# Kernel tuning notes

Hardware: AMD Instinct MI355X
Metric: run time of the kernel (lower is better)

The kernel has to match this reference:

```python
import jax, jax.numpy as jnp
import numpy as np
import math

D = 2048            # fc_feat_size (hardcoded sqrt(2048) scale in source)
IMAGES = 20         # images_per_person
NEIGHBOR = 5        # neighbor_size (sliding window width)
T = IMAGES - NEIGHBOR + 1   # number of windows = 16
SCALE = 1.0 / math.sqrt(2048.0)


def _attention(x, Wq, bq, Wk, bk, Wv, bv):
    # x: [N, L, D] -> [N, L, D]; bmm-softmax-bmm as in source
    q = x @ Wq.T + bq
    k = x @ Wk.T + bk
    v = x @ Wv.T + bv
    dot = jnp.einsum('nld,nmd->nlm', q, k) * SCALE
    w = jax.nn.softmax(dot, axis=-1)
    return jnp.einsum('nlm,nmd->nld', w, v)


def _lstm_final(x, Wih, Whh, bih, bhh):
    # PyTorch-convention LSTM (gates i,f,g,o); x: [N, L, D] -> final hidden [N, H]
    N = x.shape[0]
    H = Whh.shape[1]
    xg = x @ Wih.T + (bih + bhh)   # [N, L, 4H] precompute input projections

    def step(carry, xt):
        h, c = carry
        gates = xt + h @ Whh.T
        i, f, g, o = jnp.split(gates, 4, axis=-1)
        c = jax.nn.sigmoid(f) * c + jax.nn.sigmoid(i) * jnp.tanh(g)
        h = jax.nn.sigmoid(o) * jnp.tanh(c)
        return (h, c), None

    init = (jnp.zeros((N, H), x.dtype), jnp.zeros((N, H), x.dtype))
    (h, _), _ = jax.lax.scan(step, init, jnp.swapaxes(xg, 0, 1))
    return h


def _layernorm(x, g, b, eps=1e-5):
    mu = jnp.mean(x, axis=-1, keepdims=True)
    var = jnp.var(x, axis=-1, keepdims=True)
    return (x - mu) * jax.lax.rsqrt(var + eps) * g + b


def setup_inputs() -> dict:
    key = jax.random.key(0)
    ks = iter(jax.random.split(key, 32))
    s = 0.02
    p = {}
    p['fc_feats'] = jax.random.normal(next(ks), (64, IMAGES, D), jnp.float32)
    for pre in ('nsa', 'sa'):
        for nm in ('Wq', 'Wk', 'Wv'):
            p[f'{pre}_{nm}'] = jax.random.normal(next(ks), (D, D), jnp.float32) * s
        for nm in ('bq', 'bk', 'bv'):
            p[f'{pre}_{nm}'] = jnp.zeros((D,), jnp.float32)
        p[f'{pre}_Wih'] = jax.random.normal(next(ks), (4 * D, D), jnp.float32) * s
        p[f'{pre}_Whh'] = jax.random.normal(next(ks), (4 * D, D), jnp.float32) * s
        p[f'{pre}_bih'] = jnp.zeros((4 * D,), jnp.float32)
        p[f'{pre}_bhh'] = jnp.zeros((4 * D,), jnp.float32)
    p['ln_g'] = jnp.ones((D,), jnp.float32)
    p['ln_b'] = jnp.zeros((D,), jnp.float32)
    return p


def reference(fc_feats,
              nsa_Wq, nsa_Wk, nsa_Wv, nsa_bq, nsa_bk, nsa_bv,
              nsa_Wih, nsa_Whh, nsa_bih, nsa_bhh,
              sa_Wq, sa_Wk, sa_Wv, sa_bq, sa_bk, sa_bv,
              sa_Wih, sa_Whh, sa_bih, sa_bhh,
              ln_g, ln_b):
    B = fc_feats.shape[0]
    # Sliding windows: window t covers images [t, t+NEIGHBOR) -> [B, T, W, D]
    idx = jnp.arange(T)[:, None] + jnp.arange(NEIGHBOR)[None, :]
    windows = fc_feats[:, idx]                       # [B, T, W, D]
    wflat = windows.reshape(B * T, NEIGHBOR, D)
    # NeighboringSelfAttention: attention within window + LSTM final state
    att = _attention(wflat, nsa_Wq, nsa_bq, nsa_Wk, nsa_bk, nsa_Wv, nsa_bv)
    nsa = _lstm_final(att, nsa_Wih, nsa_Whh, nsa_bih, nsa_bhh)  # [B*T, D]
    nsa_feats = nsa.reshape(B, T, D)
    new_nsa_feats = _layernorm(nsa_feats, ln_g, ln_b)
    # SelfAttention over the T window summaries + LSTM final state
    att2 = _attention(new_nsa_feats, sa_Wq, sa_bq, sa_Wk, sa_bk, sa_Wv, sa_bv)
    sa_feats = _lstm_final(att2, sa_Wih, sa_Whh, sa_bih, sa_bhh)  # [B, D]
    return (sa_feats, new_nsa_feats)
```

## Files before the change

kernel.cpp:

```cpp
#include <hip/hip_runtime.h>
#include <hip/hip_bf16.h>

typedef unsigned int  u32;
typedef unsigned short u16;

typedef __bf16 bf16x8 __attribute__((ext_vector_type(8)));
typedef float  f32x4  __attribute__((ext_vector_type(4)));

#define D2048 2048
#define SCALE 0.022097086912079612f

__device__ __forceinline__ u32 f2bfbits(float f) {
    u32 u = __float_as_uint(f);
    return (u + 0x7FFFu + ((u >> 16) & 1u)) >> 16;
}
__device__ __forceinline__ u32 pack2(float a, float b) {
    return f2bfbits(a) | (f2bfbits(b) << 16);
}
__device__ __forceinline__ float bf2f(u32 h) {
    return __uint_as_float(h << 16);
}
__device__ __forceinline__ void unpack8(uint4 v, float* f) {
    f[0] = bf2f(v.x & 0xFFFFu); f[1] = bf2f(v.x >> 16);
    f[2] = bf2f(v.y & 0xFFFFu); f[3] = bf2f(v.y >> 16);
    f[4] = bf2f(v.z & 0xFFFFu); f[5] = bf2f(v.z >> 16);
    f[6] = bf2f(v.w & 0xFFFFu); f[7] = bf2f(v.w >> 16);
}
__device__ __forceinline__ float sigmf(float x) { return 1.f / (1.f + __expf(-x)); }
__device__ __forceinline__ float tanhf_(float x) {
    x = fminf(15.f, fmaxf(-15.f, x));
    float e = __expf(2.f * x);
    return (e - 1.f) / (e + 1.f);
}

__device__ __forceinline__ void gload_lds16(const u16* g, u16* l) {
    __builtin_amdgcn_global_load_lds(
        (const __attribute__((address_space(1))) unsigned int*)g,
        (__attribute__((address_space(3))) unsigned int*)l,
        16, 0, 0);
}

struct CvtArgs {
    const float* src[8];
    u16*         dst[8];
    int          n4[8];
    int          nseg;
};
__global__ __launch_bounds__(256) void cvt_multi(CvtArgs a) {
    int stride = gridDim.x * 256;
    for (int s = 0; s < a.nseg; ++s) {
        const float4* S = reinterpret_cast<const float4*>(a.src[s]);
        uint2*        D = reinterpret_cast<uint2*>(a.dst[s]);
        int n4 = a.n4[s];
        for (int i = blockIdx.x * 256 + threadIdx.x; i < n4; i += stride) {
            float4 v = S[i];
            uint2 p;
            p.x = pack2(v.x, v.y);
            p.y = pack2(v.z, v.w);
            D[i] = p;
        }
    }
}

template <bool QKV3, bool HAS_BIAS, bool OUT_BF16>
__global__ __launch_bounds__(256) void gemm_bt(const u16* __restrict__ A, int lda,
                                               const u16* __restrict__ B0,
                                               const u16* __restrict__ B1,
                                               const u16* __restrict__ B2,
                                               const float* __restrict__ bias0,
                                               const float* __restrict__ bias1,
                                               const float* __restrict__ bias2,
                                               void* __restrict__ Cout,
                                               size_t zCstride,
                                               int M, int N, int K) {
    __shared__ u16 Abuf[2][128 * 64];
    __shared__ u16 Bbuf[2][128 * 64];

    const int tid  = threadIdx.x;
    const int lane = tid & 63;
    const int wave = tid >> 6;
    const int wr   = (wave >> 1) * 64;
    const int wc   = (wave & 1) * 64;
    const int rowBase = blockIdx.y * 128;
    const int colBase = blockIdx.x * 128;
    const int l15 = lane & 15, l4 = lane >> 4;
    const int srow = lane >> 3;
    const int scol = (lane & 7) * 8;

    const u16* B = B0;
    const float* bias = bias0;
    void* C = Cout;
    if (QKV3) {
        int z = blockIdx.z;
        B    = (z == 0) ? B0 : ((z == 1) ? B1 : B2);
        bias = (z == 0) ? bias0 : ((z == 1) ? bias1 : bias2);
        C    = OUT_BF16 ? (void*)((u16*)Cout + (size_t)z * zCstride)
                        : (void*)((float*)Cout + (size_t)z * zCstride);
    }

    const u16* ga = A + (size_t)(rowBase + wave * 32 + srow) * lda + scol;
    const u16* gb = B + (size_t)(colBase + wave * 32 + srow) * K + scol;
    const int ldsOff = (wave * 32) * 64;

    f32x4 acc[4][4];
#pragma unroll
    for (int i = 0; i < 4; i++)
#pragma unroll
        for (int j = 0; j < 4; j++) acc[i][j] = f32x4{0.f, 0.f, 0.f, 0.f};

    const int nt = K >> 6;

#pragma unroll
    for (int i = 0; i < 4; ++i) {
        gload_lds16(ga + (size_t)(i * 8) * lda, &Abuf[0][ldsOff + i * 8 * 64]);
        gload_lds16(gb + (size_t)(i * 8) * K,   &Bbuf[0][ldsOff + i * 8 * 64]);
    }

    for (int t = 0; t < nt; ++t) {
        const int cur = t & 1;
        if (t + 1 < nt) {
            const int k1 = (t + 1) << 6;
#pragma unroll
            for (int i = 0; i < 4; ++i) {
                gload_lds16(ga + (size_t)(i * 8) * lda + k1,
                            &Abuf[cur ^ 1][ldsOff + i * 8 * 64]);
                gload_lds16(gb + (size_t)(i * 8) * K + k1,
                            &Bbuf[cur ^ 1][ldsOff + i * 8 * 64]);
            }
            asm volatile("s_waitcnt vmcnt(8)" ::: "memory");
        } else {
            asm volatile("s_waitcnt vmcnt(0)" ::: "memory");
        }
        __builtin_amdgcn_s_barrier();
        __builtin_amdgcn_sched_barrier(0);
#pragma unroll
        for (int kk = 0; kk < 2; ++kk) {
            bf16x8 af[4], bfr[4];
#pragma unroll
            for (int i = 0; i < 4; i++) {
                af[i]  = *reinterpret_cast<const bf16x8*>(
                    &Abuf[cur][(wr + i * 16 + l15) * 64 + kk * 32 + l4 * 8]);
                bfr[i] = *reinterpret_cast<const bf16x8*>(
                    &Bbuf[cur][(wc + i * 16 + l15) * 64 + kk * 32 + l4 * 8]);
            }
#pragma unroll
            for (int i = 0; i < 4; i++)
#pragma unroll
                for (int j = 0; j < 4; j++)
                    acc[i][j] = __builtin_amdgcn_mfma_f32_16x16x32_bf16(af[i], bfr[j],
                                                                        acc[i][j], 0, 0, 0);
        }
        __builtin_amdgcn_sched_barrier(0);
        __builtin_amdgcn_s_barrier();
    }

#pragma unroll
    for (int i = 0; i < 4; i++) {
        int row0 = rowBase + wr + i * 16 + l4 * 4;
#pragma unroll
        for (int j = 0; j < 4; j++) {
            int col = colBase + wc + j * 16 + l15;
            float bv = HAS_BIAS ? bias[col] : 0.f;
#pragma unroll
            for (int rr = 0; rr < 4; rr++) {
                float val = acc[i][j][rr] + bv;
                if (OUT_BF16)
                    ((u16*)C)[(size_t)(row0 + rr) * N + col] = (u16)f2bfbits(val);
                else
                    ((float*)C)[(size_t)(row0 + rr) * N + col] = val;
            }
        }
    }
}

__global__ __launch_bounds__(256) void gemm_skinny64(const u16* __restrict__ A,
                                                     const u16* __restrict__ B,
                                                     float* __restrict__ part,
                                                     int N, int K) {
    __shared__ u16 Abuf[2][64 * 64];
    __shared__ u16 Bbuf[2][128 * 64];
    const int tid = threadIdx.x, lane = tid & 63, wave = tid >> 6;
    const int colBase = blockIdx.x * 128;
    const int kp = blockIdx.y;
    const int kseg = K >> 2;
    const int kBeg = kp * kseg;
    const int l15 = lane & 15, l4 = lane >> 4;
    const int srow = lane >> 3, scol = (lane & 7) * 8;

    const u16* ga = A + (size_t)(wave * 16 + srow) * K + scol + kBeg;
    const u16* gb = B + (size_t)(colBase + wave * 32 + srow) * K + scol + kBeg;
    const int laOff = (wave * 16) * 64;
    const int lbOff = (wave * 32) * 64;

    f32x4 acc[4][2];
#pragma unroll
    for (int i = 0; i < 4; i++)
#pragma unroll
        for (int j = 0; j < 2; j++) acc[i][j] = f32x4{0.f, 0.f, 0.f, 0.f};

    const int nt = kseg >> 6;

#pragma unroll
    for (int i = 0; i < 2; ++i)
        gload_lds16(ga + (size_t)(i * 8) * K, &Abuf[0][laOff + i * 8 * 64]);
#pragma unroll
    for (int i = 0; i < 4; ++i)
        gload_lds16(gb + (size_t)(i * 8) * K, &Bbuf[0][lbOff + i * 8 * 64]);

    for (int t = 0; t < nt; ++t) {
        const int cur = t & 1;
        if (t + 1 < nt) {
            const int k1 = (t + 1) << 6;
#pragma unroll
            for (int i = 0; i < 2; ++i)
                gload_lds16(ga + (size_t)(i * 8) * K + k1, &Abuf[cur ^ 1][laOff + i * 8 * 64]);
#pragma unroll
            for (int i = 0; i < 4; ++i)
                gload_lds16(gb + (size_t)(i * 8) * K + k1, &Bbuf[cur ^ 1][lbOff + i * 8 * 64]);
            asm volatile("s_waitcnt vmcnt(6)" ::: "memory");
        } else {
            asm volatile("s_waitcnt vmcnt(0)" ::: "memory");
        }
        __builtin_amdgcn_s_barrier();
        __builtin_amdgcn_sched_barrier(0);
#pragma unroll
        for (int kk = 0; kk < 2; ++kk) {
            bf16x8 af[4], bfr[2];
#pragma unroll
            for (int i = 0; i < 4; i++)
                af[i] = *reinterpret_cast<const bf16x8*>(
                    &Abuf[cur][(i * 16 + l15) * 64 + kk * 32 + l4 * 8]);
#pragma unroll
            for (int j = 0; j < 2; j++)
                bfr[j] = *reinterpret_cast<const bf16x8*>(
                    &Bbuf[cur][(wave * 32 + j * 16 + l15) * 64 + kk * 32 + l4 * 8]);
#pragma unroll
            for (int i = 0; i < 4; i++)
#pragma unroll
                for (int j = 0; j < 2; j++)
                    acc[i][j] = __builtin_amdgcn_mfma_f32_16x16x32_bf16(af[i], bfr[j],
                                                                        acc[i][j], 0, 0, 0);
        }
        __builtin_amdgcn_sched_barrier(0);
        __builtin_amdgcn_s_barrier();
    }

    float* cp = part + (size_t)kp * 64 * N;
#pragma unroll
    for (int i = 0; i < 4; i++) {
        int row0 = i * 16 + l4 * 4;
#pragma unroll
        for (int j = 0; j < 2; j++) {
            int col = colBase + wave * 32 + j * 16 + l15;
#pragma unroll
            for (int rr = 0; rr < 4; rr++)
                cp[(size_t)(row0 + rr) * N + col] = acc[i][j][rr];
        }
    }
}

__global__ __launch_bounds__(256) void attn_win5(const u16* __restrict__ q0,
                                                 const u16* __restrict__ k0,
                                                 const u16* __restrict__ v0,
                                                 u16* __restrict__ att) {
    int n = blockIdx.x;
    int b = n >> 4, t = n & 15;
    int tid = threadIdx.x, lane = tid & 63, wave = tid >> 6;
    int d0 = tid * 8;
    size_t base = (size_t)(b * 20 + t) * D2048;

    float qv[5][8];
#pragma unroll
    for (int i = 0; i < 5; i++) {
        uint4 v = *reinterpret_cast<const uint4*>(q0 + base + (size_t)i * D2048 + d0);
        unpack8(v, qv[i]);
    }
    float part[25];
#pragma unroll
    for (int p = 0; p < 25; p++) part[p] = 0.f;
#pragma unroll
    for (int m = 0; m < 5; m++) {
        float kv[8];
        uint4 v = *reinterpret_cast<const uint4*>(k0 + base + (size_t)m * D2048 + d0);
        unpack8(v, kv);
#pragma unroll
        for (int l = 0; l < 5; l++)
#pragma unroll
            for (int j = 0; j < 8; j++) part[l * 5 + m] += qv[l][j] * kv[j];
    }
#pragma unroll
    for (int p = 0; p < 25; p++) {
        float s = part[p];
#pragma unroll
        for (int msk = 32; msk; msk >>= 1) s += __shfl_xor(s, msk, 64);
        part[p] = s;
    }
    __shared__ float wred[4][25];
    __shared__ float wmat[25];
    if (lane == 0) {
#pragma unroll
        for (int p = 0; p < 25; p++) wred[wave][p] = part[p];
    }
    __syncthreads();
    if (tid < 5) {
        int l = tid;
        float dv[5], mx = -1e30f;
#pragma unroll
        for (int m = 0; m < 5; m++) {
            dv[m] = (wred[0][l * 5 + m] + wred[1][l * 5 + m] + wred[2][l * 5 + m] +
                     wred[3][l * 5 + m]) * SCALE;
            mx = fmaxf(mx, dv[m]);
        }
        float ssum = 0.f;
#pragma unroll
        for (int m = 0; m < 5; m++) { dv[m] = __expf(dv[m] - mx); ssum += dv[m]; }
        float inv = 1.f / ssum;
#pragma unroll
        for (int m = 0; m < 5; m++) wmat[l * 5 + m] = dv[m] * inv;
    }
    __syncthreads();

    float oacc[5][8];
#pragma unroll
    for (int l = 0; l < 5; l++)
#pragma unroll
        for (int j = 0; j < 8; j++) oacc[l][j] = 0.f;
#pragma unroll
    for (int m = 0; m < 5; m++) {
        float vv[8];
        uint4 v = *reinterpret_cast<const uint4*>(v0 + base + (size_t)m * D2048 + d0);
        unpack8(v, vv);
#pragma unroll
        for (int l = 0; l < 5; l++) {
            float w = wmat[l * 5 + m];
#pragma unroll
            for (int j = 0; j < 8; j++) oacc[l][j] += w * vv[j];
        }
    }
#pragma unroll
    for (int l = 0; l < 5; l++) {
        uint4 p;
        p.x = pack2(oacc[l][0], oacc[l][1]);
        p.y = pack2(oacc[l][2], oacc[l][3]);
        p.z = pack2(oacc[l][4], oacc[l][5]);
        p.w = pack2(oacc[l][6], oacc[l][7]);
        *reinterpret_cast<uint4*>(att + (size_t)(n * 5 + l) * D2048 + d0) = p;
    }
}

__global__ __launch_bounds__(256) void attn_seq16(const u16* __restrict__ q2,
                                                  const u16* __restrict__ k2,
                                                  const u16* __restrict__ v2,
                                                  u16* __restrict__ att2) {
    int r = blockIdx.x;
    int b = r >> 4;
    int tid = threadIdx.x, lane = tid & 63, wave = tid >> 6;
    int d0 = tid * 8;
    size_t kbase = (size_t)b * 16 * D2048;

    float qv[8];
    {
        uint4 v = *reinterpret_cast<const uint4*>(q2 + (size_t)r * D2048 + d0);
        unpack8(v, qv);
    }
    float part[16];
#pragma unroll
    for (int m = 0; m < 16; m++) part[m] = 0.f;
#pragma unroll
    for (int m = 0; m < 16; m++) {
        float kv[8];
        uint4 v = *reinterpret_cast<const uint4*>(k2 + kbase + (size_t)m * D2048 + d0);
        unpack8(v, kv);
#pragma unroll
        for (int j = 0; j < 8; j++) part[m] += qv[j] * kv[j];
    }
#pragma unroll
    for (int m = 0; m < 16; m++) {
        float s = part[m];
#pragma unroll
        for (int msk = 32; msk; msk >>= 1) s += __shfl_xor(s, msk, 64);
        part[m] = s;
    }
    __shared__ float wred[4][16];
    __shared__ float wmat[16];
    if (lane == 0) {
#pragma unroll
        for (int m = 0; m < 16; m++) wred[wave][m] = part[m];
    }
    __syncthreads();
    if (tid == 0) {
        float dv[16], mx = -1e30f;
#pragma unroll
        for (int m = 0; m < 16; m++) {
            dv[m] = (wred[0][m] + wred[1][m] + wred[2][m] + wred[3][m]) * SCALE;
            mx = fmaxf(mx, dv[m]);
        }
        float ssum = 0.f;
#pragma unroll
        for (int m = 0; m < 16; m++) { dv[m] = __expf(dv[m] - mx); ssum += dv[m]; }
        float inv = 1.f / ssum;
#pragma unroll
        for (int m = 0; m < 16; m++) wmat[m] = dv[m] * inv;
    }
    __syncthreads();

    float oacc[8];
#pragma unroll
    for (int j = 0; j < 8; j++) oacc[j] = 0.f;
#pragma unroll
    for (int m = 0; m < 16; m++) {
        float vv[8];
        uint4 v = *reinterpret_cast<const uint4*>(v2 + kbase + (size_t)m * D2048 + d0);
        unpack8(v, vv);
        float w = wmat[m];
#pragma unroll
        for (int j = 0; j < 8; j++) oacc[j] += w * vv[j];
    }
    uint4 p;
    p.x = pack2(oacc[0], oacc[1]);
    p.y = pack2(oacc[2], oacc[3]);
    p.z = pack2(oacc[4], oacc[5]);
    p.w = pack2(oacc[6], oacc[7]);
    *reinterpret_cast<uint4*>(att2 + (size_t)r * D2048 + d0) = p;
}

template <int NPARTS>
__global__ __launch_bounds__(256) void lstm_gate(const u16* __restrict__ xg,
                                                 int xg_stride,
                                                 const float* __restrict__ hW,
                                                 const float* __restrict__ bih,
                                                 const float* __restrict__ bhh,
                                                 float* __restrict__ c,
                                                 float* __restrict__ h,
                                                 u16* __restrict__ hbf,
                                                 float* __restrict__ hout,
                                                 int rows) {
    int idx = blockIdx.x * 256 + threadIdx.x;
    int total = rows * 512;
    if (idx >= total) return;
    int n  = idx >> 9;
    int j4 = (idx & 511) * 4;

    const u16* xr = xg + (size_t)n * xg_stride + j4;
    float4 gi, gf, gg, go;
    {
        uint2 ri = *reinterpret_cast<const uint2*>(xr);
        uint2 rf = *reinterpret_cast<const uint2*>(xr + 2048);
        uint2 rg = *reinterpret_cast<const uint2*>(xr + 4096);
        uint2 ro = *reinterpret_cast<const uint2*>(xr + 6144);
        gi = {bf2f(ri.x & 0xFFFFu), bf2f(ri.x >> 16), bf2f(ri.y & 0xFFFFu), bf2f(ri.y >> 16)};
        gf = {bf2f(rf.x & 0xFFFFu), bf2f(rf.x >> 16), bf2f(rf.y & 0xFFFFu), bf2f(rf.y >> 16)};
        gg = {bf2f(rg.x & 0xFFFFu), bf2f(rg.x >> 16), bf2f(rg.y & 0xFFFFu), bf2f(rg.y >> 16)};
        go = {bf2f(ro.x & 0xFFFFu), bf2f(ro.x >> 16), bf2f(ro.y & 0xFFFFu), bf2f(ro.y >> 16)};
    }

    float4 bi1 = *reinterpret_cast<const float4*>(bih + j4);
    float4 bf1 = *reinterpret_cast<const float4*>(bih + 2048 + j4);
    float4 bg1 = *reinterpret_cast<const float4*>(bih + 4096 + j4);
    float4 bo1 = *reinterpret_cast<const float4*>(bih + 6144 + j4);
    float4 bi2 = *reinterpret_cast<const float4*>(bhh + j4);
    float4 bf2_ = *reinterpret_cast<const float4*>(bhh + 2048 + j4);
    float4 bg2 = *reinterpret_cast<const float4*>(bhh + 4096 + j4);
    float4 bo2 = *reinterpret_cast<const float4*>(bhh + 6144 + j4);

    gi.x += bi1.x + bi2.x; gi.y += bi1.y + bi2.y; gi.z += bi1.z + bi2.z; gi.w += bi1.w + bi2.w;
    gf.x += bf1.x + bf2_.x; gf.y += bf1.y + bf2_.y; gf.z += bf1.z + bf2_.z; gf.w += bf1.w + bf2_.w;
    gg.x += bg1.x + bg2.x; gg.y += bg1.y + bg2.y; gg.z += bg1.z + bg2.z; gg.w += bg1.w + bg2.w;
    go.x += bo1.x + bo2.x; go.y += bo1.y + bo2.y; go.z += bo1.z + bo2.z; go.w += bo1.w + bo2.w;

#pragma unroll
    for (int p = 0; p < NPARTS; ++p) {
        const float* hr = hW + (size_t)p * 524288 + (size_t)n * 8192;
        float4 hi = *reinterpret_cast<const float4*>(hr + j4);
        float4 hf = *reinterpret_cast<const float4*>(hr + 2048 + j4);
        float4 hg = *reinterpret_cast<const float4*>(hr + 4096 + j4);
        float4 ho = *reinterpret_cast<const float4*>(hr + 6144 + j4);
        gi.x += hi.x; gi.y += hi.y; gi.z += hi.z; gi.w += hi.w;
        gf.x += hf.x; gf.y += hf.y; gf.z += hf.z; gf.w += hf.w;
        gg.x += hg.x; gg.y += hg.y; gg.z += hg.z; gg.w += hg.w;
        go.x += ho.x; go.y += ho.y; go.z += ho.z; go.w += ho.w;
    }
    float4 cc;
    if (NPARTS == 0) { cc.x = cc.y = cc.z = cc.w = 0.f; }
    else             cc = *reinterpret_cast<const float4*>(c + (size_t)n * 2048 + j4);

    float cx = sigmf(gf.x) * cc.x + sigmf(gi.x) * tanhf_(gg.x);
    float cy = sigmf(gf.y) * cc.y + sigmf(gi.y) * tanhf_(gg.y);
    float cz = sigmf(gf.z) * cc.z + sigmf(gi.z) * tanhf_(gg.z);
    float cw = sigmf(gf.w) * cc.w + sigmf(gi.w) * tanhf_(gg.w);
    float hx = sigmf(go.x) * tanhf_(cx);
    float hy = sigmf(go.y) * tanhf_(cy);
    float hz = sigmf(go.z) * tanhf_(cz);
    float hw_ = sigmf(go.w) * tanhf_(cw);

    float4 co = {cx, cy, cz, cw};
    float4 ho_ = {hx, hy, hz, hw_};
    *reinterpret_cast<float4*>(c + (size_t)n * 2048 + j4) = co;
    *reinterpret_cast<float4*>(h + (size_t)n * 2048 + j4) = ho_;
    uint2 hp;
    hp.x = pack2(hx, hy);
    hp.y = pack2(hz, hw_);
    *reinterpret_cast<uint2*>(hbf + (size_t)n * 2048 + j4) = hp;
    if (hout) *reinterpret_cast<float4*>(hout + (size_t)n * 2048 + j4) = ho_;
}

__global__ __launch_bounds__(256) void layernorm_k(const float* __restrict__ x,
                                                   const float* __restrict__ g,
                                                   const float* __restrict__ b,
                                                   float* __restrict__ y,
                                                   u16* __restrict__ ybf) {
    int row = blockIdx.x;
    int tid = threadIdx.x, lane = tid & 63, wave = tid >> 6;
    const float* xr = x + (size_t)row * D2048;
    int j = tid * 8;
    float4 v1 = *reinterpret_cast<const float4*>(xr + j);
    float4 v2 = *reinterpret_cast<const float4*>(xr + j + 4);
    float s  = v1.x + v1.y + v1.z + v1.w + v2.x + v2.y + v2.z + v2.w;
    float s2 = v1.x * v1.x + v1.y * v1.y + v1.z * v1.z + v1.w * v1.w +
               v2.x * v2.x + v2.y * v2.y + v2.z * v2.z + v2.w * v2.w;
#pragma unroll
    for (int msk = 32; msk; msk >>= 1) {
        s  += __shfl_xor(s, msk, 64);
        s2 += __shfl_xor(s2, msk, 64);
    }
    __shared__ float red[4][2];
    if (lane == 0) { red[wave][0] = s; red[wave][1] = s2; }
    __syncthreads();
    s  = red[0][0] + red[1][0] + red[2][0] + red[3][0];
    s2 = red[0][1] + red[1][1] + red[2][1] + red[3][1];
    float mu  = s * (1.f / 2048.f);
    float var = s2 * (1.f / 2048.f) - mu * mu;
    float rs  = __frsqrt_rn(var + 1e-5f);

    float4 g1 = *reinterpret_cast<const float4*>(g + j);
    float4 g2 = *reinterpret_cast<const float4*>(g + j + 4);
    float4 b1 = *reinterpret_cast<const float4*>(b + j);
    float4 b2 = *reinterpret_cast<const float4*>(b + j + 4);
    float o[8];
    o[0] = (v1.x - mu) * rs * g1.x + b1.x;
    o[1] = (v1.y - mu) * rs * g1.y + b1.y;
    o[2] = (v1.z - mu) * rs * g1.z + b1.z;
    o[3] = (v1.w - mu) * rs * g1.w + b1.w;
    o[4] = (v2.x - mu) * rs * g2.x + b2.x;
    o[5] = (v2.y - mu) * rs * g2.y + b2.y;
    o[6] = (v2.z - mu) * rs * g2.z + b2.z;
    o[7] = (v2.w - mu) * rs * g2.w + b2.w;
    float4 o1 = {o[0], o[1], o[2], o[3]};
    float4 o2 = {o[4], o[5], o[6], o[7]};
    float* yr = y + (size_t)row * D2048;
    *reinterpret_cast<float4*>(yr + j)     = o1;
    *reinterpret_cast<float4*>(yr + j + 4) = o2;
    uint4 p;
    p.x = pack2(o[0], o[1]);
    p.y = pack2(o[2], o[3]);
    p.z = pack2(o[4], o[5]);
    p.w = pack2(o[6], o[7]);
    *reinterpret_cast<uint4*>(ybf + (size_t)row * D2048 + j) = p;
}

static inline void launch_gemm1(hipStream_t s, const u16* A, int lda, const u16* B,
                                void* C, int M, int N, int K, bool outbf) {
    dim3 grid(N / 128, M / 128);
    if (outbf)
        gemm_bt<false, false, true><<<grid, 256, 0, s>>>(A, lda, B, B, B,
            nullptr, nullptr, nullptr, C, 0, M, N, K);
    else
        gemm_bt<false, false, false><<<grid, 256, 0, s>>>(A, lda, B, B, B,
            nullptr, nullptr, nullptr, C, 0, M, N, K);
}

static inline void launch_qkv(hipStream_t s, const u16* A, const u16* Wq,
                              const u16* Wk, const u16* Wv, const float* bq,
                              const float* bk, const float* bv, u16* out,
                              int M, int N, int K) {
    dim3 grid(N / 128, M / 128, 3);
    gemm_bt<true, true, true><<<grid, 256, 0, s>>>(A, K, Wq, Wk, Wv, bq, bk, bv,
                                                   out, (size_t)M * N, M, N, K);
}

extern "C" void kernel_launch(void* const* d_in, const int* in_sizes, int n_in,
                              void* d_out, int out_size, void* d_ws, size_t ws_size,
                              hipStream_t stream) {
    const float* fc      = (const float*)d_in[0];
    const float* nsa_Wq  = (const float*)d_in[1];
    const float* nsa_Wk  = (const float*)d_in[2];
    const float* nsa_Wv  = (const float*)d_in[3];
    const float* nsa_bq  = (const float*)d_in[4];
    const float* nsa_bk  = (const float*)d_in[5];
    const float* nsa_bv  = (const float*)d_in[6];
    const float* nsa_Wih = (const float*)d_in[7];
    const float* nsa_Whh = (const float*)d_in[8];
    const float* nsa_bih = (const float*)d_in[9];
    const float* nsa_bhh = (const float*)d_in[10];
    const float* sa_Wq   = (const float*)d_in[11];
    const float* sa_Wk   = (const float*)d_in[12];
    const float* sa_Wv   = (const float*)d_in[13];
    const float* sa_bq   = (const float*)d_in[14];
    const float* sa_bk   = (const float*)d_in[15];
    const float* sa_bv   = (const float*)d_in[16];
    const float* sa_Wih  = (const float*)d_in[17];
    const float* sa_Whh  = (const float*)d_in[18];
    const float* sa_bih  = (const float*)d_in[19];
    const float* sa_bhh  = (const float*)d_in[20];
    const float* ln_g    = (const float*)d_in[21];
    const float* ln_b    = (const float*)d_in[22];

    float* outF   = (float*)d_out;
    float* out_sa = outF;
    float* out_ln = outF + 131072;

    char* W = (char*)d_ws;
    u16* W_q   = (u16*)(W + 0);
    u16* W_k   = (u16*)(W + 8388608);
    u16* W_v   = (u16*)(W + 16777216);
    u16* W_ih  = (u16*)(W + 25165824);
    u16* W_hh1 = (u16*)(W + 58720256);
    u16* W_hh2 = (u16*)(W + 92274688);
    u16*   Xbf  = (u16*)(W + 125829120);
    u16*   q0   = (u16*)(W + 131072000);
    u16*   att1 = (u16*)(W + 146800640);
    u16*   xg   = (u16*)(W + 167772160);
    float* h1   = (float*)(W + 0);
    float* c1   = (float*)(W + 8388608);
    u16*   h1bf = (u16*)(W + 16777216);
    float* hW1  = (float*)(W + 131072000);
    u16*   lnbf = Xbf;
    u16*   q2   = q0;
    u16*   att2 = att1;
    float* hW2  = (float*)(W + 131072000);
    float* h2   = (float*)(W + 139460608);
    float* c2   = (float*)(W + 139984896);
    u16*   h2bf = (u16*)(W + 140509184);

    {
        CvtArgs a{};
        a.src[0] = fc;      a.dst[0] = Xbf;   a.n4[0] = 655360;
        a.src[1] = nsa_Wq;  a.dst[1] = W_q;   a.n4[1] = 1048576;
        a.src[2] = nsa_Wk;  a.dst[2] = W_k;   a.n4[2] = 1048576;
        a.src[3] = nsa_Wv;  a.dst[3] = W_v;   a.n4[3] = 1048576;
        a.src[4] = nsa_Wih; a.dst[4] = W_ih;  a.n4[4] = 4194304;
        a.src[5] = nsa_Whh; a.dst[5] = W_hh1; a.n4[5] = 4194304;
        a.src[6] = sa_Whh;  a.dst[6] = W_hh2; a.n4[6] = 4194304;
        a.nseg = 7;
        cvt_multi<<<2048, 256, 0, stream>>>(a);
    }

    launch_qkv(stream, Xbf, W_q, W_k, W_v, nsa_bq, nsa_bk, nsa_bv, q0, 1280, 2048, 2048);

    attn_win5<<<1024, 256, 0, stream>>>(q0, q0 + 2621440, q0 + 5242880, att1);

    launch_gemm1(stream, att1, 2048, W_ih, xg, 5120, 8192, 2048, true);

    lstm_gate<0><<<2048, 256, 0, stream>>>(xg, 40960, nullptr, nsa_bih, nsa_bhh,
                                           c1, h1, h1bf, nullptr, 1024);
    for (int t = 1; t < 5; ++t) {
        launch_gemm1(stream, h1bf, 2048, W_hh1, hW1, 1024, 8192, 2048, false);
        lstm_gate<1><<<2048, 256, 0, stream>>>(xg + (size_t)t * 8192, 40960, hW1,
                                               nsa_bih, nsa_bhh, c1, h1, h1bf,
                                               nullptr, 1024);
    }

    layernorm_k<<<1024, 256, 0, stream>>>(h1, ln_g, ln_b, out_ln, lnbf);

    {
        CvtArgs a{};
        a.src[0] = sa_Wq;  a.dst[0] = W_q;  a.n4[0] = 1048576;
        a.src[1] = sa_Wk;  a.dst[1] = W_k;  a.n4[1] = 1048576;
        a.src[2] = sa_Wv;  a.dst[2] = W_v;  a.n4[2] = 1048576;
        a.src[3] = sa_Wih; a.dst[3] = W_ih; a.n4[3] = 4194304;
        a.nseg = 4;
        cvt_multi<<<2048, 256, 0, stream>>>(a);
    }

    launch_qkv(stream, lnbf, W_q, W_k, W_v, sa_bq, sa_bk, sa_bv, q2, 1024, 2048, 2048);

    attn_seq16<<<1024, 256, 0, stream>>>(q2, q2 + 2097152, q2 + 4194304, att2);

    launch_gemm1(stream, att2, 2048, W_ih, xg, 1024, 8192, 2048, true);

    lstm_gate<0><<<128, 256, 0, stream>>>(xg, 131072, nullptr, sa_bih, sa_bhh,
                                          c2, h2, h2bf, nullptr, 64);
    for (int t = 1; t < 16; ++t) {
        gemm_skinny64<<<dim3(64, 4), 256, 0, stream>>>(h2bf, W_hh2, hW2, 8192, 2048);
        lstm_gate<4><<<128, 256, 0, stream>>>(xg + (size_t)t * 8192, 131072, hW2,
                                              sa_bih, sa_bhh, c2, h2, h2bf,
                                              (t == 15) ? out_sa : nullptr, 64);
    }
}
```

Before: 1.077 ms.

## Add 256x256 MFMA GEMM with split-K for LSTM projections, widen skinny split

Adds a new 512-thread GEMM kernel with 256x256 tiles, XOR-swizzled LDS, direct global-to-LDS loads interleaved with MFMA phases, and optional 2-way split-K. It is used for the LSTM input projections and for the first LSTM's recurrent h@Whh GEMM, whose two split-K partials are summed in lstm_gate. The goal is higher MFMA utilisation and operand reuse than the 128x128 gemm_bt, plus more blocks for the 1024-row recurrent GEMMs. Separately, the skinny 64-row recurrent GEMM goes from 4-way to 8-way split-K, which adds more partial sums to read in the gate kernel. Workspace offsets for the second LSTM's state move so they do not overlap the new partial buffers.

New measurement: 1.030 ms. -4.4%, faster.

```diff
diff --git a/kernel.cpp b/kernel.cpp
--- a/kernel.cpp
+++ b/kernel.cpp
@@ -62,6 +62,126 @@
     }
 }
 
+template <int SPLITK, bool OUT_BF16>
+__global__ __launch_bounds__(512, 2) void gemm256(const u16* __restrict__ A, int lda,
+                                                  const u16* __restrict__ B,
+                                                  void* __restrict__ C0,
+                                                  void* __restrict__ C1,
+                                                  int M, int N, int K) {
+    __shared__ u16 Ab[2][16384];
+    __shared__ u16 Bb[2][16384];
+
+    const int tid  = threadIdx.x;
+    const int lane = tid & 63;
+    const int wid  = tid >> 6;
+    const int wm   = wid >> 2;
+    const int wn   = wid & 3;
+    const int l15  = lane & 15, l4 = lane >> 4;
+    const int rowBase = blockIdx.y * 256;
+    const int colBase = blockIdx.x * 256;
+    const int kseg = K / SPLITK;
+    const int kBeg = (SPLITK > 1) ? (int)blockIdx.z * kseg : 0;
+
+    const int srow8 = lane >> 3;
+    const int scw   = ((lane & 7) ^ srow8) * 8;
+    const u16* gA = A + (size_t)(rowBase + wid * 8 + srow8) * lda + kBeg + scw;
+    const u16* gB = B + (size_t)(colBase + wid * 8 + srow8) * (size_t)K + kBeg + scw;
+    const int ldsW = wid * 512;
+
+#define STAGE_A(buf, koff, q) \
+    gload_lds16(gA + (size_t)((q) * 64) * lda + (koff), &Ab[buf][(q) * 4096 + ldsW])
+#define STAGE_B(buf, koff, q) \
+    gload_lds16(gB + (size_t)((q) * 64) * (size_t)K + (koff), &Bb[buf][(q) * 4096 + ldsW])
+
+    f32x4 acc[8][4];
+#pragma unroll
+    for (int m = 0; m < 8; m++)
+#pragma unroll
+        for (int n = 0; n < 4; n++) acc[m][n] = f32x4{0.f, 0.f, 0.f, 0.f};
+
+    const int nt = kseg >> 6;
+
+#pragma unroll
+    for (int q = 0; q < 4; ++q) { STAGE_A(0, 0, q); STAGE_B(0, 0, q); }
+
+    const int swzA = (l15 & 7);
+
+    for (int t = 0; t < nt; ++t) {
+        const int cur = t & 1;
+        const int nxt = cur ^ 1;
+        const int kN  = (t + 1) << 6;
+        const bool more = (t + 1 < nt);
+
+        if (more) {
+            STAGE_A(nxt, kN, 0);
+            STAGE_A(nxt, kN, 1);
+            asm volatile("s_waitcnt vmcnt(2)" ::: "memory");
+        } else {
+            asm volatile("s_waitcnt vmcnt(0)" ::: "memory");
+        }
+        __builtin_amdgcn_s_barrier();
+
+        bf16x8 bfrag[4][2];
+#pragma unroll
+        for (int n = 0; n < 4; ++n)
+#pragma unroll
+            for (int kk = 0; kk < 2; ++kk)
+                bfrag[n][kk] = *reinterpret_cast<const bf16x8*>(
+                    &Bb[cur][(wn * 64 + n * 16 + l15) * 64 +
+                             (((kk * 4 + l4) ^ swzA) * 8)]);
+
+#pragma unroll
+        for (int p = 0; p < 4; ++p) {
+            bf16x8 afr[2][2];
+#pragma unroll
+            for (int mi = 0; mi < 2; ++mi)
+#pragma unroll
+                for (int kk = 0; kk < 2; ++kk)
+                    afr[mi][kk] = *reinterpret_cast<const bf16x8*>(
+                        &Ab[cur][(wm * 128 + (p * 2 + mi) * 16 + l15) * 64 +
+                                 (((kk * 4 + l4) ^ swzA) * 8)]);
+            if (more) {
+                if (p == 0)      { STAGE_A(nxt, kN, 2); STAGE_A(nxt, kN, 3); }
+                else if (p == 1) { STAGE_B(nxt, kN, 0); STAGE_B(nxt, kN, 1); }
+                else if (p == 2) { STAGE_B(nxt, kN, 2); STAGE_B(nxt, kN, 3); }
+            }
+            __builtin_amdgcn_s_barrier();
+            __builtin_amdgcn_sched_barrier(0);
+            __builtin_amdgcn_s_setprio(1);
+#pragma unroll
+            for (int kk = 0; kk < 2; ++kk)
+#pragma unroll
+                for (int mi = 0; mi < 2; ++mi)
+#pragma unroll
+                    for (int n = 0; n < 4; ++n)
+                        acc[p * 2 + mi][n] = __builtin_amdgcn_mfma_f32_16x16x32_bf16(
+                            afr[mi][kk], bfrag[n][kk], acc[p * 2 + mi][n], 0, 0, 0);
+            __builtin_amdgcn_s_setprio(0);
+            __builtin_amdgcn_sched_barrier(0);
+            __builtin_amdgcn_s_barrier();
+        }
+    }
+#undef STAGE_A
+#undef STAGE_B
+
+    float* fdst = (SPLITK > 1 && blockIdx.z) ? (float*)C1 : (float*)C0;
+#pragma unroll
+    for (int m = 0; m < 8; ++m) {
+        int row0 = rowBase + wm * 128 + m * 16 + l4 * 4;
+#pragma unroll
+        for (int n = 0; n < 4; ++n) {
+            int col = colBase + wn * 64 + n * 16 + l15;
+#pragma unroll
+            for (int rr = 0; rr < 4; ++rr) {
+                if (OUT_BF16)
+                    ((u16*)C0)[(size_t)(row0 + rr) * N + col] = (u16)f2bfbits(acc[m][n][rr]);
+                else
+                    fdst[(size_t)(row0 + rr) * N + col] = acc[m][n][rr];
+            }
+        }
+    }
+}
+
 template <bool QKV3, bool HAS_BIAS, bool OUT_BF16>
 __global__ __launch_bounds__(256) void gemm_bt(const u16* __restrict__ A, int lda,
                                                const u16* __restrict__ B0,
@@ -182,7 +302,7 @@
     const int tid = threadIdx.x, lane = tid & 63, wave = tid >> 6;
     const int colBase = blockIdx.x * 128;
     const int kp = blockIdx.y;
-    const int kseg = K >> 2;
+    const int kseg = K >> 3;
     const int kBeg = kp * kseg;
     const int l15 = lane & 15, l4 = lane >> 4;
     const int srow = lane >> 3, scol = (lane & 7) * 8;
@@ -427,7 +547,8 @@
 template <int NPARTS>
 __global__ __launch_bounds__(256) void lstm_gate(const u16* __restrict__ xg,
                                                  int xg_stride,
-                                                 const float* __restrict__ hW,
+                                                 const float* __restrict__ hWa,
+                                                 const float* __restrict__ hWb,
                                                  const float* __restrict__ bih,
                                                  const float* __restrict__ bhh,
                                                  float* __restrict__ c,
@@ -470,7 +591,9 @@
 
 #pragma unroll
     for (int p = 0; p < NPARTS; ++p) {
-        const float* hr = hW + (size_t)p * 524288 + (size_t)n * 8192;
+        const float* hr = (NPARTS == 2)
+            ? ((p == 0 ? hWa : hWb) + (size_t)n * 8192)
+            : (hWa + (size_t)p * 524288 + (size_t)n * 8192);
         float4 hi = *reinterpret_cast<const float4*>(hr + j4);
         float4 hf = *reinterpret_cast<const float4*>(hr + 2048 + j4);
         float4 hg = *reinterpret_cast<const float4*>(hr + 4096 + j4);
@@ -556,17 +679,6 @@
     p.z = pack2(o[4], o[5]);
     p.w = pack2(o[6], o[7]);
     *reinterpret_cast<uint4*>(ybf + (size_t)row * D2048 + j) = p;
-}
-
-static inline void launch_gemm1(hipStream_t s, const u16* A, int lda, const u16* B,
-                                void* C, int M, int N, int K, bool outbf) {
-    dim3 grid(N / 128, M / 128);
-    if (outbf)
-        gemm_bt<false, false, true><<<grid, 256, 0, s>>>(A, lda, B, B, B,
-            nullptr, nullptr, nullptr, C, 0, M, N, K);
-    else
-        gemm_bt<false, false, false><<<grid, 256, 0, s>>>(A, lda, B, B, B,
-            nullptr, nullptr, nullptr, C, 0, M, N, K);
 }
 
 static inline void launch_qkv(hipStream_t s, const u16* A, const u16* Wq,
@@ -623,14 +735,15 @@
     float* h1   = (float*)(W + 0);
     float* c1   = (float*)(W + 8388608);
     u16*   h1bf = (u16*)(W + 16777216);
-    float* hW1  = (float*)(W + 131072000);
+    float* partA = (float*)(W + 131072000);
+    float* partB = (float*)(W + 25165824);
     u16*   lnbf = Xbf;
     u16*   q2   = q0;
     u16*   att2 = att1;
     float* hW2  = (float*)(W + 131072000);
-    float* h2   = (float*)(W + 139460608);
-    float* c2   = (float*)(W + 139984896);
-    u16*   h2bf = (u16*)(W + 140509184);
+    float* h2   = (float*)(W + 147849216);
+    float* c2   = (float*)(W + 148373504);
+    u16*   h2bf = (u16*)(W + 148897792);
 
     {
         CvtArgs a{};
@@ -649,14 +762,16 @@
 
     attn_win5<<<1024, 256, 0, stream>>>(q0, q0 + 2621440, q0 + 5242880, att1);
 
-    launch_gemm1(stream, att1, 2048, W_ih, xg, 5120, 8192, 2048, true);
-
-    lstm_gate<0><<<2048, 256, 0, stream>>>(xg, 40960, nullptr, nsa_bih, nsa_bhh,
-                                           c1, h1, h1bf, nullptr, 1024);
+    gemm256<1, true><<<dim3(32, 20, 1), 512, 0, stream>>>(att1, 2048, W_ih,
+                                                          xg, nullptr, 5120, 8192, 2048);
+
+    lstm_gate<0><<<2048, 256, 0, stream>>>(xg, 40960, nullptr, nullptr, nsa_bih,
+                                           nsa_bhh, c1, h1, h1bf, nullptr, 1024);
     for (int t = 1; t < 5; ++t) {
-        launch_gemm1(stream, h1bf, 2048, W_hh1, hW1, 1024, 8192, 2048, false);
-        lstm_gate<1><<<2048, 256, 0, stream>>>(xg + (size_t)t * 8192, 40960, hW1,
-                                               nsa_bih, nsa_bhh, c1, h1, h1bf,
+        gemm256<2, false><<<dim3(32, 4, 2), 512, 0, stream>>>(h1bf, 2048, W_hh1,
+                                                              partA, partB, 1024, 8192, 2048);
+        lstm_gate<2><<<2048, 256, 0, stream>>>(xg + (size_t)t * 8192, 40960, partA,
+                                               partB, nsa_bih, nsa_bhh, c1, h1, h1bf,
                                                nullptr, 1024);
     }
 
@@ -676,14 +791,15 @@
 
     attn_seq16<<<1024, 256, 0, stream>>>(q2, q2 + 2097152, q2 + 4194304, att2);
 
-    launch_gemm1(stream, att2, 2048, W_ih, xg, 1024, 8192, 2048, true);
-
-    lstm_gate<0><<<128, 256, 0, stream>>>(xg, 131072, nullptr, sa_bih, sa_bhh,
-                                          c2, h2, h2bf, nullptr, 64);
+    gemm256<1, true><<<dim3(32, 4, 1), 512, 0, stream>>>(att2, 2048, W_ih,
+                                                         xg, nullptr, 1024, 8192, 2048);
+
+    lstm_gate<0><<<128, 256, 0, stream>>>(xg, 131072, nullptr, nullptr, sa_bih,
+                                          sa_bhh, c2, h2, h2bf, nullptr, 64);
     for (int t = 1; t < 16; ++t) {
-        gemm_skinny64<<<dim3(64, 4), 256, 0, stream>>>(h2bf, W_hh2, hW2, 8192, 2048);
-        lstm_gate<4><<<128, 256, 0, stream>>>(xg + (size_t)t * 8192, 131072, hW2,
-                                              sa_bih, sa_bhh, c2, h2, h2bf,
+        gemm_skinny64<<<dim3(64, 8), 256, 0, stream>>>(h2bf, W_hh2, hW2, 8192, 2048);
+        lstm_gate<8><<<128, 256, 0, stream>>>(xg + (size_t)t * 8192, 131072, hW2,
+                                              nullptr, sa_bih, sa_bhh, c2, h2, h2bf,
                                               (t == 15) ? out_sa : nullptr, 64);
     }
 }
```
